# Optimization experiments

Measured on AMD Instinct MI355X. Metric: run time of the kernel, lower is better.

The kernel has to match this reference:

```python
import jax, jax.numpy as jnp
import numpy as np

N_NODES = 32768
N_EDGES = 524288
NODE_DIM = 128
HIDDEN = 256
EDGE_DIM = 32


def setup_inputs() -> dict:
    key = jax.random.key(0)
    ks = jax.random.split(key, 12)
    s = 0.05
    return {
        "h": jax.random.normal(ks[0], (N_NODES, NODE_DIM), jnp.float32),
        "x": jax.random.normal(ks[1], (N_NODES, 3), jnp.float32) * 10.0,
        "edge_index": jax.random.randint(ks[2], (2, N_EDGES), 0, N_NODES, dtype=jnp.int32).astype(jnp.int64),
        "edge_dist": jax.random.uniform(ks[3], (N_EDGES,), jnp.float32) * 15.0,
        # edge_mlp: Linear(1, edge_dim) -> SiLU -> Linear(edge_dim, edge_dim)
        "We1": jax.random.normal(ks[4], (1, EDGE_DIM), jnp.float32) * s,
        "be1": jnp.zeros((EDGE_DIM,), jnp.float32),
        "We2": jax.random.normal(ks[5], (EDGE_DIM, EDGE_DIM), jnp.float32) * s,
        "be2": jnp.zeros((EDGE_DIM,), jnp.float32),
        # node_mlp: Linear(2*node+edge, hidden) -> SiLU -> Linear(hidden, node)
        "Wn1": jax.random.normal(ks[6], (2 * NODE_DIM + EDGE_DIM, HIDDEN), jnp.float32) * s,
        "bn1": jnp.zeros((HIDDEN,), jnp.float32),
        "Wn2": jax.random.normal(ks[7], (HIDDEN, NODE_DIM), jnp.float32) * s,
        "bn2": jnp.zeros((NODE_DIM,), jnp.float32),
        # coord_mlp: Linear(2*node+edge, hidden) -> SiLU -> Linear(hidden, 1, bias=False)
        "Wc1": jax.random.normal(ks[8], (2 * NODE_DIM + EDGE_DIM, HIDDEN), jnp.float32) * s,
        "bc1": jnp.zeros((HIDDEN,), jnp.float32),
        "Wc2": jax.random.normal(ks[9], (HIDDEN, 1), jnp.float32) * s,
    }


def reference(h, x, edge_index, edge_dist,
              We1, be1, We2, be2,
              Wn1, bn1, Wn2, bn2,
              Wc1, bc1, Wc2):
    src, dst = edge_index[0], edge_index[1]
    n_nodes = h.shape[0]

    # edge_mlp on scalar distances -> [E, edge_dim]
    edge_attr = jax.nn.silu(edge_dist[:, None] @ We1 + be1) @ We2 + be2

    # per-edge message input: [E, 2*node_dim + edge_dim]
    m_input = jnp.concatenate([h[src], h[dst], edge_attr], axis=-1)

    # node messages and scatter-add onto destination nodes
    m = jax.nn.silu(m_input @ Wn1 + bn1) @ Wn2 + bn2          # [E, node_dim]
    h_agg = jax.ops.segment_sum(m, dst, num_segments=n_nodes)  # [N, node_dim]

    # equivariant coordinate update along normalized edge direction
    coord_weight = jax.nn.silu(m_input @ Wc1 + bc1) @ Wc2      # [E, 1]
    dir_vec = x[src] - x[dst]                                  # [E, 3]
    dir_len = jnp.maximum(jnp.linalg.norm(dir_vec, axis=-1, keepdims=True), 1e-8)
    coord_update = coord_weight * (dir_vec / dir_len)          # [E, 3]
    x_agg = jax.ops.segment_sum(coord_update, dst, num_segments=n_nodes)

    return h + h_agg, x + x_agg
```

## Files before the change

kernel.cpp:

```cpp
#include <hip/hip_runtime.h>
#include <math.h>

#define N_NODES 32768
#define N_EDGES 524288
#define NODE_DIM 128
#define HIDDEN 256
#define EDGE_DIM 32
#define TE 32
#define NBLK (N_EDGES / TE)
#define ASTR 296
#define HSTR 264
#define MSTR 132

typedef __attribute__((ext_vector_type(8))) short bf16x8;
typedef __attribute__((ext_vector_type(16))) float f32x16;

__device__ __forceinline__ float silu_f(float v) {
    float e = __expf(-v);
    return v * __builtin_amdgcn_rcpf(1.0f + e);
}

__device__ __forceinline__ unsigned short f2bf_rne(float f) {
    union { float f; unsigned int u; } v; v.f = f;
    return (unsigned short)((v.u + 0x7fffu + ((v.u >> 16) & 1u)) >> 16);
}
__device__ __forceinline__ unsigned int pk_rne(float a, float b) {
    return (unsigned int)f2bf_rne(a) | ((unsigned int)f2bf_rne(b) << 16);
}
__device__ __forceinline__ unsigned int pkbf(float a, float b) {
    union { float f; unsigned int u; } ua, ub; ua.f = a; ub.f = b;
    return __builtin_amdgcn_perm(ub.u + 0x8000u, ua.u + 0x8000u, 0x07060302u);
}
__device__ __forceinline__ unsigned short f2bf_hu(float f) {
    union { float f; unsigned int u; } v; v.f = f;
    return (unsigned short)((v.u + 0x8000u) >> 16);
}

__device__ __forceinline__ int detect_is64(const void* ei, int t) {
    const unsigned int* ew = (const unsigned int*)ei;
    unsigned int hiw = ew[2 * (t & 63) + 1];
    return (__ballot(hiw != 0u) == 0ULL) ? 1 : 0;
}

#define WS_BIAS_OFF 1024
#define WS_W1S_OFF  69632
#define WS_W2S_OFF  364544
#define WS_CNT_OFF  430080
#define WS_CUR_OFF  561152
#define WS_PERM_OFF 692224
#define WS_PART_OFF 2789376
#define WS_HBF_OFF  2790400
#define WS_HBF_END  (WS_HBF_OFF + N_NODES * NODE_DIM * 2)

#define SEG_HIST 524288
#define SEG_W1S  147456
#define SEG_W2S  32768
#define SEG_BIAS 512
#define SEG_OUT  1073152
#define SEG_HBF  524288
#define PREP_TOT (SEG_HIST + SEG_W1S + SEG_W2S + SEG_BIAS + SEG_OUT + SEG_HBF)

__global__ void prep_hist_kernel(const float* __restrict__ h, const float* __restrict__ x,
                                 const void* __restrict__ ei,
                                 const float* __restrict__ We2, const float* __restrict__ be2,
                                 const float* __restrict__ Wn1, const float* __restrict__ bn1,
                                 const float* __restrict__ Wn2,
                                 const float* __restrict__ Wc1, const float* __restrict__ bc1,
                                 float* __restrict__ out, float* __restrict__ biasC,
                                 unsigned short* __restrict__ W1s, unsigned short* __restrict__ W2s,
                                 int* __restrict__ counts, unsigned short* __restrict__ hbf) {
    int i = blockIdx.x * 256 + threadIdx.x;
    if (i < SEG_HIST) {
        int is64 = detect_is64(ei, threadIdx.x);
        int dst = is64 ? (int)((const long long*)ei)[N_EDGES + i]
                       : ((const int*)ei)[N_EDGES + i];
        atomicAdd(&counts[dst], 1);
        return;
    }
    i -= SEG_HIST;
    if (i < SEG_W1S) {
        int jj = i & 7, ln = (i >> 3) & 63, rest = i >> 9;
        int step = rest % 18, tile = rest / 18;
        int n = tile * 32 + (ln & 31);
        int k = step * 16 + ((ln >> 5) * 8) + jj;
        float v;
        if (k < 256) {
            v = (n < 256) ? Wn1[k * 256 + n] : Wc1[k * 256 + (n - 256)];
        } else {
            int j = k - 256;
            float s = 0.0f;
            #pragma unroll 8
            for (int q = 0; q < 32; ++q)
                s += We2[j * 32 + q] * ((n < 256) ? Wn1[(256 + q) * 256 + n]
                                                  : Wc1[(256 + q) * 256 + (n - 256)]);
            v = s;
        }
        W1s[i] = f2bf_rne(v);
        return;
    }
    i -= SEG_W1S;
    if (i < SEG_W2S) {
        int jj = i & 7, ln = (i >> 3) & 63, rest = i >> 9;
        int step = rest & 15, tile = rest >> 4;
        int d = tile * 32 + (ln & 31);
        int k = step * 16 + ((ln >> 5) * 8) + jj;
        W2s[i] = f2bf_rne(Wn2[k * 128 + d]);
        return;
    }
    i -= SEG_W2S;
    if (i < SEG_BIAS) {
        int n = i;
        float s = (n < 256) ? bn1[n] : bc1[n - 256];
        #pragma unroll 8
        for (int q = 0; q < 32; ++q)
            s += be2[q] * ((n < 256) ? Wn1[(256 + q) * 256 + n]
                                     : Wc1[(256 + q) * 256 + (n - 256)]);
        biasC[n] = s;
        return;
    }
    i -= SEG_BIAS;
    if (i < SEG_OUT) {
        const int NH4 = N_NODES * NODE_DIM / 4;
        const float4* h4 = (const float4*)h;
        const float4* x4 = (const float4*)x;
        ((float4*)out)[i] = (i < NH4) ? h4[i] : x4[i - NH4];
        return;
    }
    i -= SEG_OUT;
    if (hbf != nullptr && i < SEG_HBF) {
        const float4* p = (const float4*)&h[i * 8];
        float4 v0 = p[0], v1 = p[1];
        uint4 o = make_uint4(pk_rne(v0.x, v0.y), pk_rne(v0.z, v0.w),
                             pk_rne(v1.x, v1.y), pk_rne(v1.z, v1.w));
        *(uint4*)&hbf[i * 8] = o;
    }
}

__global__ __launch_bounds__(256)
void scan_fused_kernel(const int* __restrict__ counts, int* __restrict__ cursor) {
    __shared__ int pb[128];
    __shared__ int loc[256];
    const int t = threadIdx.x;
    const int b = blockIdx.x;
    if (t < 128) {
        const int4* c4 = (const int4*)(counts + t * 256);
        int s = 0;
        #pragma unroll 8
        for (int i = 0; i < 64; ++i) { int4 v = c4[i]; s += v.x + v.y + v.z + v.w; }
        pb[t] = s;
    }
    int c = counts[b * 256 + t];
    loc[t] = c;
    __syncthreads();
    if (t == 0) {
        int s = 0;
        for (int j = 0; j < 128; ++j) { int v = pb[j]; pb[j] = s; s += v; }
    }
    #pragma unroll
    for (int d = 1; d < 256; d <<= 1) {
        int v = (t >= d) ? loc[t - d] : 0;
        __syncthreads();
        loc[t] += v;
        __syncthreads();
    }
    cursor[b * 256 + t] = pb[b] + loc[t] - c;
}

__global__ void place_kernel(const void* __restrict__ ei,
                             int* __restrict__ cursor, int* __restrict__ perm) {
    int is64 = detect_is64(ei, threadIdx.x);
    int e = blockIdx.x * 256 + threadIdx.x;
    int dst = is64 ? (int)((const long long*)ei)[N_EDGES + e]
                   : ((const int*)ei)[N_EDGES + e];
    int pos = atomicAdd(&cursor[dst], 1);
    perm[pos] = e;
}

__global__ __launch_bounds__(256, 6)
void egnn_mfma_kernel(const float* __restrict__ h, const float* __restrict__ x,
                      const void* __restrict__ ei, const float* __restrict__ dist,
                      const float* __restrict__ We1, const float* __restrict__ be1,
                      const float* __restrict__ bn2, const float* __restrict__ Wc2,
                      const float* __restrict__ biasC,
                      const unsigned short* __restrict__ W1s,
                      const unsigned short* __restrict__ W2s,
                      const int* __restrict__ perm,
                      const unsigned short* __restrict__ hbf,
                      float* __restrict__ out)
{
    __shared__ unsigned short smA[TE * ASTR];
    __shared__ int sidx[TE], didx[TE], eidx[TE];
    __shared__ float cw_s[TE];
    __shared__ float cxyz[3 * TE];

    unsigned short* smH = smA;
    float* smM = (float*)smA;

    const int t = threadIdx.x;
    const int lane = t & 63;
    const int wv = t >> 6;
    const int lo = lane & 31;
    const int hi = lane >> 5;
    const int swz = ((blockIdx.x & 7) * (NBLK / 8)) + (blockIdx.x >> 3);
    const int ebase = swz * TE;
    const int is64 = detect_is64(ei, t);

    if (t < 2 * TE) {
        int e = t & (TE - 1);
        int eid = perm[ebase + e];
        int which = t >> 5;
        long long pos = (long long)which * N_EDGES + eid;
        int idx = is64 ? (int)((const long long*)ei)[pos] : ((const int*)ei)[pos];
        if (which == 0) { sidx[e] = idx; eidx[e] = eid; }
        else didx[e] = idx;
        if (t < TE) cw_s[t] = 0.0f;
    }
    __syncthreads();

    if (hbf != nullptr) {
        #pragma unroll
        for (int it = 0; it < 4; ++it) {
            int id = it * 256 + t;
            int g = id & 15;
            int half = (id >> 4) & 1;
            int e = id >> 5;
            int node = half ? didx[e] : sidx[e];
            uint4 v = *(const uint4*)&hbf[node * NODE_DIM + 8 * g];
            *(uint4*)&smA[e * ASTR + half * NODE_DIM + 8 * g] = v;
        }
    } else {
        #pragma unroll
        for (int it = 0; it < 4; ++it) {
            int id = it * 256 + t;
            int g8 = id & 15;
            int half = (id >> 4) & 1;
            int e = id >> 5;
            int node = half ? didx[e] : sidx[e];
            const float4* p = (const float4*)&h[node * NODE_DIM + 8 * g8];
            float4 v0 = p[0], v1 = p[1];
            unsigned int a0 = pkbf(v0.x, v0.y), a1 = pkbf(v0.z, v0.w);
            unsigned int a2 = pkbf(v1.x, v1.y), a3 = pkbf(v1.z, v1.w);
            *(uint4*)&smA[e * ASTR + half * NODE_DIM + 8 * g8] = make_uint4(a0, a1, a2, a3);
        }
    }
    {
        int e = t >> 3;
        int j4 = (t & 7) * 4;
        float d = dist[eidx[e]];
        float s0 = silu_f(d * We1[j4 + 0] + be1[j4 + 0]);
        float s1 = silu_f(d * We1[j4 + 1] + be1[j4 + 1]);
        float s2 = silu_f(d * We1[j4 + 2] + be1[j4 + 2]);
        float s3 = silu_f(d * We1[j4 + 3] + be1[j4 + 3]);
        *(uint2*)&smA[e * ASTR + 2 * NODE_DIM + j4] = make_uint2(pkbf(s0, s1), pkbf(s2, s3));
    }
    if (t < TE) {
        int s = sidx[t], dn = didx[t];
        float dx = x[s * 3 + 0] - x[dn * 3 + 0];
        float dy = x[s * 3 + 1] - x[dn * 3 + 1];
        float dz = x[s * 3 + 2] - x[dn * 3 + 2];
        float len = fmaxf(sqrtf(dx * dx + dy * dy + dz * dz), 1e-8f);
        float inv = 1.0f / len;
        cxyz[t] = dx * inv; cxyz[TE + t] = dy * inv; cxyz[2 * TE + t] = dz * inv;
    }
    __syncthreads();

    const int rowbase = 4 * hi;

    {
        f32x16 c0, c1;
        {
            float b0 = biasC[256 + wv * 32 + lo];
            float b1 = biasC[256 + (wv + 4) * 32 + lo];
            #pragma unroll
            for (int r = 0; r < 16; ++r) { c0[r] = b0; c1[r] = b1; }
        }
        {
            const int ao = lo * ASTR + hi * 8;
            const int TS = 18 * 64 * 8;
            const int q0 = (8 + wv) * TS + lane * 8;
            const int q1 = (12 + wv) * TS + lane * 8;
            bf16x8 p0[2], p1[2];
            p0[0] = *(const bf16x8*)&W1s[q0];
            p1[0] = *(const bf16x8*)&W1s[q1];
            #pragma unroll
            for (int step = 0; step < 18; ++step) {
                const int cur = step & 1, nxt = cur ^ 1;
                if (step + 1 < 18) {
                    p0[nxt] = *(const bf16x8*)&W1s[q0 + (step + 1) * 512];
                    p1[nxt] = *(const bf16x8*)&W1s[q1 + (step + 1) * 512];
                }
                bf16x8 f = *(const bf16x8*)&smA[ao + step * 16];
                c0 = __builtin_amdgcn_mfma_f32_32x32x16_bf16(f, p0[cur], c0, 0, 0, 0);
                c1 = __builtin_amdgcn_mfma_f32_32x32x16_bf16(f, p1[cur], c1, 0, 0, 0);
            }
        }
        float w0 = Wc2[wv * 32 + lo];
        float w1 = Wc2[(wv + 4) * 32 + lo];
        float p[16];
        #pragma unroll
        for (int r = 0; r < 16; ++r)
            p[r] = silu_f(c0[r]) * w0 + silu_f(c1[r]) * w1;
        #pragma unroll
        for (int off = 1; off < 32; off <<= 1) {
            #pragma unroll
            for (int r = 0; r < 16; ++r) p[r] += __shfl_xor(p[r], off);
        }
        if (lo == 0) {
            #pragma unroll
            for (int r = 0; r < 16; ++r)
                atomicAdd(&cw_s[(r & 3) + 8 * (r >> 2) + rowbase], p[r]);
        }
    }

    f32x16 a0, a1;
    {
        float b0 = biasC[wv * 32 + lo];
        float b1 = biasC[(wv + 4) * 32 + lo];
        #pragma unroll
        for (int r = 0; r < 16; ++r) { a0[r] = b0; a1[r] = b1; }
        const int ao = lo * ASTR + hi * 8;
        const int TS = 18 * 64 * 8;
        const int q0 = (wv) * TS + lane * 8;
        const int q1 = (wv + 4) * TS + lane * 8;
        bf16x8 p0[2], p1[2];
        p0[0] = *(const bf16x8*)&W1s[q0];
        p1[0] = *(const bf16x8*)&W1s[q1];
        #pragma unroll
        for (int step = 0; step < 18; ++step) {
            const int cur = step & 1, nxt = cur ^ 1;
            if (step + 1 < 18) {
                p0[nxt] = *(const bf16x8*)&W1s[q0 + (step + 1) * 512];
                p1[nxt] = *(const bf16x8*)&W1s[q1 + (step + 1) * 512];
            }
            bf16x8 f = *(const bf16x8*)&smA[ao + step * 16];
            a0 = __builtin_amdgcn_mfma_f32_32x32x16_bf16(f, p0[cur], a0, 0, 0, 0);
            a1 = __builtin_amdgcn_mfma_f32_32x32x16_bf16(f, p1[cur], a1, 0, 0, 0);
        }
    }
    __syncthreads();

    {
        const int jb0 = (wv    ) * 32 + lo;
        const int jb1 = (wv + 4) * 32 + lo;
        #pragma unroll
        for (int r = 0; r < 16; ++r) {
            int er = (r & 3) + 8 * (r >> 2) + rowbase;
            smH[er * HSTR + jb0] = f2bf_hu(silu_f(a0[r]));
            smH[er * HSTR + jb1] = f2bf_hu(silu_f(a1[r]));
        }
    }
    if (t < TE) {
        float w = cw_s[t];
        cxyz[t] *= w; cxyz[TE + t] *= w; cxyz[2 * TE + t] *= w;
    }
    __syncthreads();

    {
        const int d = wv * 32 + lo;
        f32x16 acc;
        float bb = bn2[d];
        #pragma unroll
        for (int r = 0; r < 16; ++r) acc[r] = bb;
        const int hoff = lo * HSTR + hi * 8;
        const int wb = wv * (16 * 64 * 8) + lane * 8;
        bf16x8 bs[2];
        bs[0] = *(const bf16x8*)&W2s[wb];
        #pragma unroll
        for (int step = 0; step < 16; ++step) {
            const int cur = step & 1, nxt = cur ^ 1;
            if (step + 1 < 16)
                bs[nxt] = *(const bf16x8*)&W2s[wb + (step + 1) * 512];
            bf16x8 af = *(const bf16x8*)&smH[hoff + step * 16];
            acc = __builtin_amdgcn_mfma_f32_32x32x16_bf16(af, bs[cur], acc, 0, 0, 0);
        }
        __syncthreads();
        #pragma unroll
        for (int r = 0; r < 16; ++r) {
            int er = (r & 3) + 8 * (r >> 2) + rowbase;
            smM[er * MSTR + d] = acc[r];
        }
    }
    __syncthreads();

    {
        const int g = t >> 5;
        const int d4 = (t & 31) * 4;
        for (int e0 = g; e0 < TE; e0 += 8) {
            if (e0 > 0 && didx[e0] == didx[e0 - 1]) continue;
            float4 s = *(const float4*)&smM[e0 * MSTR + d4];
            int er = e0 + 1;
            while (er < TE && didx[er] == didx[e0]) {
                float4 v = *(const float4*)&smM[er * MSTR + d4];
                s.x += v.x; s.y += v.y; s.z += v.z; s.w += v.w;
                ++er;
            }
            float* dp = &out[didx[e0] * NODE_DIM + d4];
            if (e0 > 0 && er < TE) {
                float4 cur = *(const float4*)dp;
                cur.x += s.x; cur.y += s.y; cur.z += s.z; cur.w += s.w;
                *(float4*)dp = cur;
            } else {
                atomicAdd(dp + 0, s.x); atomicAdd(dp + 1, s.y);
                atomicAdd(dp + 2, s.z); atomicAdd(dp + 3, s.w);
            }
        }
    }
    if (t < TE) {
        int e0 = t;
        if (e0 == 0 || didx[e0] != didx[e0 - 1]) {
            float sx = cxyz[e0], sy = cxyz[TE + e0], sz = cxyz[2 * TE + e0];
            int er = e0 + 1;
            while (er < TE && didx[er] == didx[e0]) {
                sx += cxyz[er]; sy += cxyz[TE + er]; sz += cxyz[2 * TE + er];
                ++er;
            }
            float* xo = out + N_NODES * NODE_DIM + didx[e0] * 3;
            if (e0 > 0 && er < TE) {
                xo[0] += sx; xo[1] += sy; xo[2] += sz;
            } else {
                atomicAdd(xo + 0, sx); atomicAdd(xo + 1, sy); atomicAdd(xo + 2, sz);
            }
        }
    }
}

extern "C" void kernel_launch(void* const* d_in, const int* in_sizes, int n_in,
                              void* d_out, int out_size, void* d_ws, size_t ws_size,
                              hipStream_t stream) {
    const float* h    = (const float*)d_in[0];
    const float* x    = (const float*)d_in[1];
    const void*  ei   = d_in[2];
    const float* dist = (const float*)d_in[3];
    const float* We1  = (const float*)d_in[4];
    const float* be1  = (const float*)d_in[5];
    const float* We2  = (const float*)d_in[6];
    const float* be2  = (const float*)d_in[7];
    const float* Wn1  = (const float*)d_in[8];
    const float* bn1  = (const float*)d_in[9];
    const float* Wn2  = (const float*)d_in[10];
    const float* bn2  = (const float*)d_in[11];
    const float* Wc1  = (const float*)d_in[12];
    const float* bc1  = (const float*)d_in[13];
    const float* Wc2  = (const float*)d_in[14];
    float* out = (float*)d_out;

    float* biasC = (float*)((char*)d_ws + WS_BIAS_OFF);
    unsigned short* W1s = (unsigned short*)((char*)d_ws + WS_W1S_OFF);
    unsigned short* W2s = (unsigned short*)((char*)d_ws + WS_W2S_OFF);
    int* counts   = (int*)((char*)d_ws + WS_CNT_OFF);
    int* cursor   = (int*)((char*)d_ws + WS_CUR_OFF);
    int* perm     = (int*)((char*)d_ws + WS_PERM_OFF);
    unsigned short* hbf = (ws_size >= (size_t)WS_HBF_END)
                        ? (unsigned short*)((char*)d_ws + WS_HBF_OFF) : nullptr;

    hipMemsetAsync(counts, 0, N_NODES * sizeof(int), stream);

    prep_hist_kernel<<<PREP_TOT / 256, 256, 0, stream>>>(
        h, x, ei, We2, be2, Wn1, bn1, Wn2, Wc1, bc1,
        out, biasC, W1s, W2s, counts, hbf);

    scan_fused_kernel<<<128, 256, 0, stream>>>(counts, cursor);
    place_kernel<<<N_EDGES / 256, 256, 0, stream>>>(ei, cursor, perm);

    egnn_mfma_kernel<<<NBLK, 256, 0, stream>>>(
        h, x, ei, dist, We1, be1, bn2, Wc2, biasC, W1s, W2s, perm, hbf, out);
}
```

Baseline: 467.9 us.

## Double edge tile to 64 per block so each wave reuses weights across two edge tiles

Each block now processes 64 edges with 512 threads instead of 32 edges with 256 threads. In both first-layer GEMMs, each wave now owns one 32-column weight slice and applies it to two 32-edge row tiles, rather than two weight slices applied to one edge tile. This halves the weight-fragment global/L2 traffic per edge and reduces the number of blocks. The cost is larger LDS usage per block and a stricter register and occupancy budget at 512 threads; the second GEMM and the scatter loop are remapped to cover the doubled edge count.

```diff
diff --git a/kernel.cpp b/kernel.cpp
--- a/kernel.cpp
+++ b/kernel.cpp
@@ -6,7 +6,7 @@
 #define NODE_DIM 128
 #define HIDDEN 256
 #define EDGE_DIM 32
-#define TE 32
+#define TE 64
 #define NBLK (N_EDGES / TE)
 #define ASTR 296
 #define HSTR 264
@@ -48,7 +48,6 @@
 #define WS_CNT_OFF  430080
 #define WS_CUR_OFF  561152
 #define WS_PERM_OFF 692224
-#define WS_PART_OFF 2789376
 #define WS_HBF_OFF  2790400
 #define WS_HBF_END  (WS_HBF_OFF + N_NODES * NODE_DIM * 2)
 
@@ -176,7 +175,7 @@
     perm[pos] = e;
 }
 
-__global__ __launch_bounds__(256, 6)
+__global__ __launch_bounds__(512, 6)
 void egnn_mfma_kernel(const float* __restrict__ h, const float* __restrict__ x,
                       const void* __restrict__ ei, const float* __restrict__ dist,
                       const float* __restrict__ We1, const float* __restrict__ be1,
@@ -208,7 +207,7 @@
     if (t < 2 * TE) {
         int e = t & (TE - 1);
         int eid = perm[ebase + e];
-        int which = t >> 5;
+        int which = t >> 6;
         long long pos = (long long)which * N_EDGES + eid;
         int idx = is64 ? (int)((const long long*)ei)[pos] : ((const int*)ei)[pos];
         if (which == 0) { sidx[e] = idx; eidx[e] = eid; }
@@ -220,7 +219,7 @@
     if (hbf != nullptr) {
         #pragma unroll
         for (int it = 0; it < 4; ++it) {
-            int id = it * 256 + t;
+            int id = it * 512 + t;
             int g = id & 15;
             int half = (id >> 4) & 1;
             int e = id >> 5;
@@ -231,7 +230,7 @@
     } else {
         #pragma unroll
         for (int it = 0; it < 4; ++it) {
-            int id = it * 256 + t;
+            int id = it * 512 + t;
             int g8 = id & 15;
             int half = (id >> 4) & 1;
             int e = id >> 5;
@@ -265,88 +264,85 @@
     __syncthreads();
 
     const int rowbase = 4 * hi;
+    const int aoff0 = lo * ASTR + hi * 8;
+    const int aoff1 = (32 + lo) * ASTR + hi * 8;
+    const int TS = 18 * 64 * 8;
 
     {
         f32x16 c0, c1;
         {
-            float b0 = biasC[256 + wv * 32 + lo];
-            float b1 = biasC[256 + (wv + 4) * 32 + lo];
+            float b = biasC[256 + wv * 32 + lo];
             #pragma unroll
-            for (int r = 0; r < 16; ++r) { c0[r] = b0; c1[r] = b1; }
+            for (int r = 0; r < 16; ++r) { c0[r] = b; c1[r] = b; }
         }
         {
-            const int ao = lo * ASTR + hi * 8;
-            const int TS = 18 * 64 * 8;
-            const int q0 = (8 + wv) * TS + lane * 8;
-            const int q1 = (12 + wv) * TS + lane * 8;
-            bf16x8 p0[2], p1[2];
-            p0[0] = *(const bf16x8*)&W1s[q0];
-            p1[0] = *(const bf16x8*)&W1s[q1];
+            const int q = (8 + wv) * TS + lane * 8;
+            bf16x8 p[2];
+            p[0] = *(const bf16x8*)&W1s[q];
             #pragma unroll
             for (int step = 0; step < 18; ++step) {
                 const int cur = step & 1, nxt = cur ^ 1;
-                if (step + 1 < 18) {
-                    p0[nxt] = *(const bf16x8*)&W1s[q0 + (step + 1) * 512];
-                    p1[nxt] = *(const bf16x8*)&W1s[q1 + (step + 1) * 512];
-                }
-                bf16x8 f = *(const bf16x8*)&smA[ao + step * 16];
-                c0 = __builtin_amdgcn_mfma_f32_32x32x16_bf16(f, p0[cur], c0, 0, 0, 0);
-                c1 = __builtin_amdgcn_mfma_f32_32x32x16_bf16(f, p1[cur], c1, 0, 0, 0);
-            }
-        }
-        float w0 = Wc2[wv * 32 + lo];
-        float w1 = Wc2[(wv + 4) * 32 + lo];
-        float p[16];
-        #pragma unroll
-        for (int r = 0; r < 16; ++r)
-            p[r] = silu_f(c0[r]) * w0 + silu_f(c1[r]) * w1;
+                if (step + 1 < 18)
+                    p[nxt] = *(const bf16x8*)&W1s[q + (step + 1) * 512];
+                bf16x8 f0 = *(const bf16x8*)&smA[aoff0 + step * 16];
+                bf16x8 f1 = *(const bf16x8*)&smA[aoff1 + step * 16];
+                c0 = __builtin_amdgcn_mfma_f32_32x32x16_bf16(f0, p[cur], c0, 0, 0, 0);
+                c1 = __builtin_amdgcn_mfma_f32_32x32x16_bf16(f1, p[cur], c1, 0, 0, 0);
+            }
+        }
+        float w = Wc2[wv * 32 + lo];
+        float p0[16], p1[16];
+        #pragma unroll
+        for (int r = 0; r < 16; ++r) {
+            p0[r] = silu_f(c0[r]) * w;
+            p1[r] = silu_f(c1[r]) * w;
+        }
         #pragma unroll
         for (int off = 1; off < 32; off <<= 1) {
             #pragma unroll
-            for (int r = 0; r < 16; ++r) p[r] += __shfl_xor(p[r], off);
+            for (int r = 0; r < 16; ++r) {
+                p0[r] += __shfl_xor(p0[r], off);
+                p1[r] += __shfl_xor(p1[r], off);
+            }
         }
         if (lo == 0) {
             #pragma unroll
-            for (int r = 0; r < 16; ++r)
-                atomicAdd(&cw_s[(r & 3) + 8 * (r >> 2) + rowbase], p[r]);
+            for (int r = 0; r < 16; ++r) {
+                int er = (r & 3) + 8 * (r >> 2) + rowbase;
+                atomicAdd(&cw_s[er], p0[r]);
+                atomicAdd(&cw_s[er + 32], p1[r]);
+            }
         }
     }
 
     f32x16 a0, a1;
     {
-        float b0 = biasC[wv * 32 + lo];
-        float b1 = biasC[(wv + 4) * 32 + lo];
-        #pragma unroll
-        for (int r = 0; r < 16; ++r) { a0[r] = b0; a1[r] = b1; }
-        const int ao = lo * ASTR + hi * 8;
-        const int TS = 18 * 64 * 8;
-        const int q0 = (wv) * TS + lane * 8;
-        const int q1 = (wv + 4) * TS + lane * 8;
-        bf16x8 p0[2], p1[2];
-        p0[0] = *(const bf16x8*)&W1s[q0];
-        p1[0] = *(const bf16x8*)&W1s[q1];
+        float b = biasC[wv * 32 + lo];
+        #pragma unroll
+        for (int r = 0; r < 16; ++r) { a0[r] = b; a1[r] = b; }
+        const int q = wv * TS + lane * 8;
+        bf16x8 p[2];
+        p[0] = *(const bf16x8*)&W1s[q];
         #pragma unroll
         for (int step = 0; step < 18; ++step) {
             const int cur = step & 1, nxt = cur ^ 1;
-            if (step + 1 < 18) {
-                p0[nxt] = *(const bf16x8*)&W1s[q0 + (step + 1) * 512];
-                p1[nxt] = *(const bf16x8*)&W1s[q1 + (step + 1) * 512];
-            }
-            bf16x8 f = *(const bf16x8*)&smA[ao + step * 16];
-            a0 = __builtin_amdgcn_mfma_f32_32x32x16_bf16(f, p0[cur], a0, 0, 0, 0);
-            a1 = __builtin_amdgcn_mfma_f32_32x32x16_bf16(f, p1[cur], a1, 0, 0, 0);
-        }
-    }
-    __syncthreads();
-
-    {
-        const int jb0 = (wv    ) * 32 + lo;
-        const int jb1 = (wv + 4) * 32 + lo;
+            if (step + 1 < 18)
+                p[nxt] = *(const bf16x8*)&W1s[q + (step + 1) * 512];
+            bf16x8 f0 = *(const bf16x8*)&smA[aoff0 + step * 16];
+            bf16x8 f1 = *(const bf16x8*)&smA[aoff1 + step * 16];
+            a0 = __builtin_amdgcn_mfma_f32_32x32x16_bf16(f0, p[cur], a0, 0, 0, 0);
+            a1 = __builtin_amdgcn_mfma_f32_32x32x16_bf16(f1, p[cur], a1, 0, 0, 0);
+        }
+    }
+    __syncthreads();
+
+    {
+        const int jb = wv * 32 + lo;
         #pragma unroll
         for (int r = 0; r < 16; ++r) {
             int er = (r & 3) + 8 * (r >> 2) + rowbase;
-            smH[er * HSTR + jb0] = f2bf_hu(silu_f(a0[r]));
-            smH[er * HSTR + jb1] = f2bf_hu(silu_f(a1[r]));
+            smH[(er     ) * HSTR + jb] = f2bf_hu(silu_f(a0[r]));
+            smH[(er + 32) * HSTR + jb] = f2bf_hu(silu_f(a1[r]));
         }
     }
     if (t < TE) {
@@ -356,13 +352,15 @@
     __syncthreads();
 
     {
-        const int d = wv * 32 + lo;
+        const int et = wv >> 2;
+        const int dt = wv & 3;
+        const int d = dt * 32 + lo;
         f32x16 acc;
         float bb = bn2[d];
         #pragma unroll
         for (int r = 0; r < 16; ++r) acc[r] = bb;
-        const int hoff = lo * HSTR + hi * 8;
-        const int wb = wv * (16 * 64 * 8) + lane * 8;
+        const int hoff = (et * 32 + lo) * HSTR + hi * 8;
+        const int wb = dt * (16 * 64 * 8) + lane * 8;
         bf16x8 bs[2];
         bs[0] = *(const bf16x8*)&W2s[wb];
         #pragma unroll
@@ -376,7 +374,7 @@
         __syncthreads();
         #pragma unroll
         for (int r = 0; r < 16; ++r) {
-            int er = (r & 3) + 8 * (r >> 2) + rowbase;
+            int er = et * 32 + (r & 3) + 8 * (r >> 2) + rowbase;
             smM[er * MSTR + d] = acc[r];
         }
     }
@@ -385,7 +383,7 @@
     {
         const int g = t >> 5;
         const int d4 = (t & 31) * 4;
-        for (int e0 = g; e0 < TE; e0 += 8) {
+        for (int e0 = g; e0 < TE; e0 += 16) {
             if (e0 > 0 && didx[e0] == didx[e0 - 1]) continue;
             float4 s = *(const float4*)&smM[e0 * MSTR + d4];
             int er = e0 + 1;
@@ -462,6 +460,6 @@
     scan_fused_kernel<<<128, 256, 0, stream>>>(counts, cursor);
     place_kernel<<<N_EDGES / 256, 256, 0, stream>>>(ei, cursor, perm);
 
-    egnn_mfma_kernel<<<NBLK, 256, 0, stream>>>(
+    egnn_mfma_kernel<<<NBLK, 512, 0, stream>>>(
         h, x, ei, dist, We1, be1, bn2, Wc2, biasC, W1s, W2s, perm, hbf, out);
 }
```

After: 465.0 us. Within noise of the previous version (-0.6%).
